# Performance work log

Hardware: AMD Instinct MI355X
Metric: run time of the kernel (lower is better)

Reference implementation:

```python
import jax, jax.numpy as jnp
import numpy as np

B, L, D = 8, 2048, 64

def setup_inputs() -> dict:
    key = jax.random.key(0)
    k1, k2 = jax.random.split(key)
    query = jax.random.normal(k1, (B, L, D), dtype=jnp.float32)
    key_t = jax.random.normal(k2, (B, L, D), dtype=jnp.float32)
    return {"query": query, "key": key_t}

def reference(query, key):
    d = query.shape[-1]
    # scores: [B, Lq, Lk] = Q K^T / sqrt(d)
    scores = jnp.einsum('bqd,bkd->bqk', query, key) / jnp.sqrt(jnp.asarray(d, query.dtype))
    weights = jax.nn.softmax(scores, axis=-1)  # dropout p=0.0 -> identity
    # output uses `key` as values, matching the original module
    return jnp.einsum('bqk,bkd->bqd', weights, key)
```

## Files before the change

### kernel.cpp

```cpp
#include <hip/hip_runtime.h>
#include <hip/hip_bf16.h>


#define LL 2048
#define DD 64
#define BQ 128
#define BK 64
#define KPAD 72
#define NSEG 8

typedef __attribute__((ext_vector_type(8))) short bf16x8;
typedef __attribute__((ext_vector_type(4))) float f32x4;

static __device__ __forceinline__ unsigned short f2bf(float f) {
  unsigned u = __builtin_bit_cast(unsigned, f);
  u += 0x7fffu + ((u >> 16) & 1u);
  return (unsigned short)(u >> 16);
}

__global__ __launch_bounds__(256, 4) void attn_kernel(
    const float* __restrict__ Q, const float* __restrict__ K,
    float* __restrict__ O, float* __restrict__ Opart,
    float* __restrict__ Lp, int seglen, int nseg) {
  __shared__ __attribute__((aligned(16))) unsigned short sKt[BK][KPAD];
  __shared__ __attribute__((aligned(16))) unsigned short sKtT[DD * KPAD];
  __shared__ __attribute__((aligned(16))) unsigned short sP[4][32][KPAD];

  const int tid  = threadIdx.x;
  const int wave = tid >> 6;
  const int lane = tid & 63;
  const int quad = lane >> 4;
  const int l16  = lane & 15;

  const int batch = blockIdx.y;
  const int seg   = blockIdx.z;
  const int q0w   = blockIdx.x * BQ + wave * 32;
  const int BLrows = gridDim.y * LL;

  const float qs = 0.125f * 1.44269504f;
  bf16x8 aq[2][2];
#pragma unroll
  for (int qb = 0; qb < 2; ++qb) {
    const float* qrow = Q + (size_t)(batch * LL + q0w + qb * 16 + l16) * DD;
#pragma unroll
    for (int ks = 0; ks < 2; ++ks) {
      const float* p = qrow + ks * 32 + quad * 8;
      float4 f0 = *(const float4*)(p);
      float4 f1 = *(const float4*)(p + 4);
      bf16x8 a;
      a[0] = (short)f2bf(f0.x * qs); a[1] = (short)f2bf(f0.y * qs);
      a[2] = (short)f2bf(f0.z * qs); a[3] = (short)f2bf(f0.w * qs);
      a[4] = (short)f2bf(f1.x * qs); a[5] = (short)f2bf(f1.y * qs);
      a[6] = (short)f2bf(f1.z * qs); a[7] = (short)f2bf(f1.w * qs);
      aq[qb][ks] = a;
    }
  }

  f32x4 oacc[2][4];
  float l_part[2][4];
#pragma unroll
  for (int qb = 0; qb < 2; ++qb) {
#pragma unroll
    for (int n = 0; n < 4; ++n) oacc[qb][n] = (f32x4){0.f, 0.f, 0.f, 0.f};
#pragma unroll
    for (int r = 0; r < 4; ++r) l_part[qb][r] = 0.f;
  }

  const int niter = seglen / BK;
  for (int t = 0; t < niter; ++t) {
    const int kv0 = seg * seglen + t * BK;
    __syncthreads();

    const float4* ksrc = (const float4*)(K + (size_t)(batch * LL + kv0) * DD);
#pragma unroll
    for (int i = 0; i < 2; ++i) {
      int p  = tid + i * 256;
      int kv = p >> 3;
      int a  = p & 7;
      float4 f0 = ksrc[p * 2];
      float4 f1 = ksrc[p * 2 + 1];
      unsigned short h[8];
      h[0] = f2bf(f0.x); h[1] = f2bf(f0.y); h[2] = f2bf(f0.z); h[3] = f2bf(f0.w);
      h[4] = f2bf(f1.x); h[5] = f2bf(f1.y); h[6] = f2bf(f1.z); h[7] = f2bf(f1.w);
      *(bf16x8*)&sKt[kv][a * 8] = *(const bf16x8*)h;
      int swz = (((kv >> 3) ^ a) & 7) * 8 + (kv & 7);
      unsigned short* dst = &sKtT[(a * 8) * KPAD + swz];
#pragma unroll
      for (int j = 0; j < 8; ++j) dst[j * KPAD] = h[j];
    }
    __syncthreads();

    f32x4 s0[4], s1[4];
#pragma unroll
    for (int n = 0; n < 4; ++n) {
      bf16x8 b0 = *(const bf16x8*)&sKt[n * 16 + l16][0 * 32 + quad * 8];
      bf16x8 b1 = *(const bf16x8*)&sKt[n * 16 + l16][1 * 32 + quad * 8];
      f32x4 z = (f32x4){0.f, 0.f, 0.f, 0.f};
      s0[n] = __builtin_amdgcn_mfma_f32_16x16x32_bf16(aq[0][0], b0, z, 0, 0, 0);
      s0[n] = __builtin_amdgcn_mfma_f32_16x16x32_bf16(aq[0][1], b1, s0[n], 0, 0, 0);
      s1[n] = __builtin_amdgcn_mfma_f32_16x16x32_bf16(aq[1][0], b0, z, 0, 0, 0);
      s1[n] = __builtin_amdgcn_mfma_f32_16x16x32_bf16(aq[1][1], b1, s1[n], 0, 0, 0);
    }

#pragma unroll
    for (int n = 0; n < 4; ++n) {
#pragma unroll
      for (int r = 0; r < 4; ++r) {
        float p0 = __builtin_amdgcn_exp2f(s0[n][r]);
        float p1 = __builtin_amdgcn_exp2f(s1[n][r]);
        l_part[0][r] += p0;
        l_part[1][r] += p1;
        sP[wave][quad * 4 + r][n * 16 + l16] = f2bf(p0);
        sP[wave][16 + quad * 4 + r][n * 16 + l16] = f2bf(p1);
      }
    }

#pragma unroll
    for (int ks = 0; ks < 2; ++ks) {
      bf16x8 a0 = *(const bf16x8*)&sP[wave][l16][ks * 32 + quad * 8];
      bf16x8 a1 = *(const bf16x8*)&sP[wave][16 + l16][ks * 32 + quad * 8];
#pragma unroll
      for (int n2 = 0; n2 < 4; ++n2) {
        int d = n2 * 16 + l16;
        bf16x8 b = *(const bf16x8*)&sKtT[d * KPAD + (((ks * 4 + quad) ^ (d >> 3)) & 7) * 8];
        oacc[0][n2] = __builtin_amdgcn_mfma_f32_16x16x32_bf16(a0, b, oacc[0][n2], 0, 0, 0);
        oacc[1][n2] = __builtin_amdgcn_mfma_f32_16x16x32_bf16(a1, b, oacc[1][n2], 0, 0, 0);
      }
    }
  }

#pragma unroll
  for (int qb = 0; qb < 2; ++qb)
#pragma unroll
    for (int r = 0; r < 4; ++r)
#pragma unroll
      for (int off = 1; off < 16; off <<= 1)
        l_part[qb][r] += __shfl_xor(l_part[qb][r], off);

  if (nseg == 1) {
#pragma unroll
    for (int qb = 0; qb < 2; ++qb)
#pragma unroll
      for (int r = 0; r < 4; ++r) {
        float invl = 1.0f / l_part[qb][r];
        float* orow = O + (size_t)(batch * LL + q0w + qb * 16 + quad * 4 + r) * DD;
#pragma unroll
        for (int n2 = 0; n2 < 4; ++n2)
          orow[n2 * 16 + l16] = oacc[qb][n2][r] * invl;
      }
  } else {
#pragma unroll
    for (int qb = 0; qb < 2; ++qb)
#pragma unroll
      for (int r = 0; r < 4; ++r) {
        int row = batch * LL + q0w + qb * 16 + quad * 4 + r;
        float* op = Opart + ((size_t)seg * BLrows + row) * DD;
#pragma unroll
        for (int n2 = 0; n2 < 4; ++n2)
          op[n2 * 16 + l16] = oacc[qb][n2][r];
        if (l16 == 0) Lp[seg * BLrows + row] = l_part[qb][r];
      }
  }
}

__global__ __launch_bounds__(256) void combine_kernel(
    const float* __restrict__ Opart, const float* __restrict__ Lp,
    float* __restrict__ O, int nseg, int BLrows) {
  const int tid = threadIdx.x;
  const int row = blockIdx.x * 4 + (tid >> 6);
  const int d   = tid & 63;
  float denom = 0.f, acc = 0.f;
  for (int s = 0; s < nseg; ++s) {
    denom += Lp[s * BLrows + row];
    acc   += Opart[((size_t)s * BLrows + row) * DD + d];
  }
  O[(size_t)row * DD + d] = acc / denom;
}

extern "C" void kernel_launch(void* const* d_in, const int* in_sizes, int n_in,
                              void* d_out, int out_size, void* d_ws, size_t ws_size,
                              hipStream_t stream) {
  const float* Q = (const float*)d_in[0];
  const float* K = (const float*)d_in[1];
  float* O = (float*)d_out;
  int B = in_sizes[0] / (LL * DD);
  int BLrows = B * LL;

  size_t need = ((size_t)NSEG * BLrows * DD + (size_t)NSEG * BLrows) * sizeof(float);
  if (ws_size >= need) {
    float* Opart = (float*)d_ws;
    float* Lpp = Opart + (size_t)NSEG * BLrows * DD;
    dim3 grid(LL / BQ, B, NSEG);
    attn_kernel<<<grid, 256, 0, stream>>>(Q, K, O, Opart, Lpp, LL / NSEG, NSEG);
    combine_kernel<<<dim3(BLrows / 4), 256, 0, stream>>>(Opart, Lpp, O, NSEG, BLrows);
  } else {
    dim3 grid(LL / BQ, B, 1);
    attn_kernel<<<grid, 256, 0, stream>>>(Q, K, O, nullptr, nullptr, LL, 1);
  }
}
```

Before: 91.56 us.

## Prefetch K tiles into registers, transpose score MFMA, store bf16 partials

Loads for the next K tile now go into registers while the current tile is being converted into shared memory, so global latency overlaps with compute. The score MFMA operands are swapped so each lane holds four consecutive keys for one query. This allows vectorized 8-byte writes of P to LDS and a cheaper row-sum reduction with only two shuffles. Split-K partial outputs are written as bf16 instead of fp32, halving the workspace traffic between the attention and combine kernels, at some cost in accuracy.

```diff
diff --git a/kernel.cpp b/kernel.cpp
--- a/kernel.cpp
+++ b/kernel.cpp
@@ -11,16 +11,21 @@
 
 typedef __attribute__((ext_vector_type(8))) short bf16x8;
 typedef __attribute__((ext_vector_type(4))) float f32x4;
+typedef __attribute__((ext_vector_type(4))) unsigned short u16x4;
 
 static __device__ __forceinline__ unsigned short f2bf(float f) {
   unsigned u = __builtin_bit_cast(unsigned, f);
   u += 0x7fffu + ((u >> 16) & 1u);
   return (unsigned short)(u >> 16);
 }
+static __device__ __forceinline__ float bf2f(unsigned short h) {
+  unsigned u = (unsigned)h << 16;
+  return __builtin_bit_cast(float, u);
+}
 
 __global__ __launch_bounds__(256, 4) void attn_kernel(
     const float* __restrict__ Q, const float* __restrict__ K,
-    float* __restrict__ O, float* __restrict__ Opart,
+    float* __restrict__ O, unsigned short* __restrict__ Opart,
     float* __restrict__ Lp, int seglen, int nseg) {
   __shared__ __attribute__((aligned(16))) unsigned short sKt[BK][KPAD];
   __shared__ __attribute__((aligned(16))) unsigned short sKtT[DD * KPAD];
@@ -38,10 +43,10 @@
   const int BLrows = gridDim.y * LL;
 
   const float qs = 0.125f * 1.44269504f;
-  bf16x8 aq[2][2];
-#pragma unroll
-  for (int qb = 0; qb < 2; ++qb) {
-    const float* qrow = Q + (size_t)(batch * LL + q0w + qb * 16 + l16) * DD;
+  bf16x8 bq[2][2];
+#pragma unroll
+  for (int qt = 0; qt < 2; ++qt) {
+    const float* qrow = Q + (size_t)(batch * LL + q0w + qt * 16 + l16) * DD;
 #pragma unroll
     for (int ks = 0; ks < 2; ++ks) {
       const float* p = qrow + ks * 32 + quad * 8;
@@ -52,66 +57,85 @@
       a[2] = (short)f2bf(f0.z * qs); a[3] = (short)f2bf(f0.w * qs);
       a[4] = (short)f2bf(f1.x * qs); a[5] = (short)f2bf(f1.y * qs);
       a[6] = (short)f2bf(f1.z * qs); a[7] = (short)f2bf(f1.w * qs);
-      aq[qb][ks] = a;
+      bq[qt][ks] = a;
     }
   }
 
   f32x4 oacc[2][4];
-  float l_part[2][4];
-#pragma unroll
-  for (int qb = 0; qb < 2; ++qb) {
-#pragma unroll
-    for (int n = 0; n < 4; ++n) oacc[qb][n] = (f32x4){0.f, 0.f, 0.f, 0.f};
-#pragma unroll
-    for (int r = 0; r < 4; ++r) l_part[qb][r] = 0.f;
+  float l_part[2];
+#pragma unroll
+  for (int qt = 0; qt < 2; ++qt) {
+#pragma unroll
+    for (int n = 0; n < 4; ++n) oacc[qt][n] = (f32x4){0.f, 0.f, 0.f, 0.f};
+    l_part[qt] = 0.f;
   }
 
   const int niter = seglen / BK;
+  const float4* kseg = (const float4*)(K + (size_t)(batch * LL + seg * seglen) * DD);
+
+  float4 pf[2][2];
+#pragma unroll
+  for (int i = 0; i < 2; ++i) {
+    int p = tid + i * 256;
+    pf[i][0] = kseg[p * 2];
+    pf[i][1] = kseg[p * 2 + 1];
+  }
+
   for (int t = 0; t < niter; ++t) {
-    const int kv0 = seg * seglen + t * BK;
     __syncthreads();
 
-    const float4* ksrc = (const float4*)(K + (size_t)(batch * LL + kv0) * DD);
 #pragma unroll
     for (int i = 0; i < 2; ++i) {
       int p  = tid + i * 256;
       int kv = p >> 3;
-      int a  = p & 7;
-      float4 f0 = ksrc[p * 2];
-      float4 f1 = ksrc[p * 2 + 1];
+      int oc = p & 7;
       unsigned short h[8];
-      h[0] = f2bf(f0.x); h[1] = f2bf(f0.y); h[2] = f2bf(f0.z); h[3] = f2bf(f0.w);
-      h[4] = f2bf(f1.x); h[5] = f2bf(f1.y); h[6] = f2bf(f1.z); h[7] = f2bf(f1.w);
-      *(bf16x8*)&sKt[kv][a * 8] = *(const bf16x8*)h;
-      int swz = (((kv >> 3) ^ a) & 7) * 8 + (kv & 7);
-      unsigned short* dst = &sKtT[(a * 8) * KPAD + swz];
+      h[0] = f2bf(pf[i][0].x); h[1] = f2bf(pf[i][0].y);
+      h[2] = f2bf(pf[i][0].z); h[3] = f2bf(pf[i][0].w);
+      h[4] = f2bf(pf[i][1].x); h[5] = f2bf(pf[i][1].y);
+      h[6] = f2bf(pf[i][1].z); h[7] = f2bf(pf[i][1].w);
+      *(bf16x8*)&sKt[kv][oc * 8] = *(const bf16x8*)h;
+      int swz = (((kv >> 3) ^ oc) & 7) * 8 + (kv & 7);
+      unsigned short* dst = &sKtT[(oc * 8) * KPAD + swz];
 #pragma unroll
       for (int j = 0; j < 8; ++j) dst[j * KPAD] = h[j];
     }
+
+    if (t + 1 < niter) {
+      const float4* ksrc = kseg + (t + 1) * (BK * DD / 4);
+#pragma unroll
+      for (int i = 0; i < 2; ++i) {
+        int p = tid + i * 256;
+        pf[i][0] = ksrc[p * 2];
+        pf[i][1] = ksrc[p * 2 + 1];
+      }
+    }
     __syncthreads();
 
-    f32x4 s0[4], s1[4];
-#pragma unroll
-    for (int n = 0; n < 4; ++n) {
-      bf16x8 b0 = *(const bf16x8*)&sKt[n * 16 + l16][0 * 32 + quad * 8];
-      bf16x8 b1 = *(const bf16x8*)&sKt[n * 16 + l16][1 * 32 + quad * 8];
+    f32x4 s[2][4];
+#pragma unroll
+    for (int mt = 0; mt < 4; ++mt) {
+      bf16x8 k0 = *(const bf16x8*)&sKt[mt * 16 + l16][quad * 8];
+      bf16x8 k1 = *(const bf16x8*)&sKt[mt * 16 + l16][32 + quad * 8];
       f32x4 z = (f32x4){0.f, 0.f, 0.f, 0.f};
-      s0[n] = __builtin_amdgcn_mfma_f32_16x16x32_bf16(aq[0][0], b0, z, 0, 0, 0);
-      s0[n] = __builtin_amdgcn_mfma_f32_16x16x32_bf16(aq[0][1], b1, s0[n], 0, 0, 0);
-      s1[n] = __builtin_amdgcn_mfma_f32_16x16x32_bf16(aq[1][0], b0, z, 0, 0, 0);
-      s1[n] = __builtin_amdgcn_mfma_f32_16x16x32_bf16(aq[1][1], b1, s1[n], 0, 0, 0);
-    }
-
-#pragma unroll
-    for (int n = 0; n < 4; ++n) {
-#pragma unroll
-      for (int r = 0; r < 4; ++r) {
-        float p0 = __builtin_amdgcn_exp2f(s0[n][r]);
-        float p1 = __builtin_amdgcn_exp2f(s1[n][r]);
-        l_part[0][r] += p0;
-        l_part[1][r] += p1;
-        sP[wave][quad * 4 + r][n * 16 + l16] = f2bf(p0);
-        sP[wave][16 + quad * 4 + r][n * 16 + l16] = f2bf(p1);
+      s[0][mt] = __builtin_amdgcn_mfma_f32_16x16x32_bf16(k0, bq[0][0], z, 0, 0, 0);
+      s[0][mt] = __builtin_amdgcn_mfma_f32_16x16x32_bf16(k1, bq[0][1], s[0][mt], 0, 0, 0);
+      s[1][mt] = __builtin_amdgcn_mfma_f32_16x16x32_bf16(k0, bq[1][0], z, 0, 0, 0);
+      s[1][mt] = __builtin_amdgcn_mfma_f32_16x16x32_bf16(k1, bq[1][1], s[1][mt], 0, 0, 0);
+    }
+
+#pragma unroll
+    for (int qt = 0; qt < 2; ++qt) {
+#pragma unroll
+      for (int mt = 0; mt < 4; ++mt) {
+        u16x4 h;
+#pragma unroll
+        for (int r = 0; r < 4; ++r) {
+          float p = __builtin_amdgcn_exp2f(s[qt][mt][r]);
+          l_part[qt] += p;
+          h[r] = f2bf(p);
+        }
+        *(u16x4*)&sP[wave][qt * 16 + l16][mt * 16 + quad * 4] = h;
       }
     }
 
@@ -120,51 +144,52 @@
       bf16x8 a0 = *(const bf16x8*)&sP[wave][l16][ks * 32 + quad * 8];
       bf16x8 a1 = *(const bf16x8*)&sP[wave][16 + l16][ks * 32 + quad * 8];
 #pragma unroll
-      for (int n2 = 0; n2 < 4; ++n2) {
-        int d = n2 * 16 + l16;
+      for (int nt = 0; nt < 4; ++nt) {
+        int d = nt * 16 + l16;
         bf16x8 b = *(const bf16x8*)&sKtT[d * KPAD + (((ks * 4 + quad) ^ (d >> 3)) & 7) * 8];
-        oacc[0][n2] = __builtin_amdgcn_mfma_f32_16x16x32_bf16(a0, b, oacc[0][n2], 0, 0, 0);
-        oacc[1][n2] = __builtin_amdgcn_mfma_f32_16x16x32_bf16(a1, b, oacc[1][n2], 0, 0, 0);
-      }
-    }
-  }
-
-#pragma unroll
-  for (int qb = 0; qb < 2; ++qb)
-#pragma unroll
-    for (int r = 0; r < 4; ++r)
-#pragma unroll
-      for (int off = 1; off < 16; off <<= 1)
-        l_part[qb][r] += __shfl_xor(l_part[qb][r], off);
+        oacc[0][nt] = __builtin_amdgcn_mfma_f32_16x16x32_bf16(a0, b, oacc[0][nt], 0, 0, 0);
+        oacc[1][nt] = __builtin_amdgcn_mfma_f32_16x16x32_bf16(a1, b, oacc[1][nt], 0, 0, 0);
+      }
+    }
+  }
+
+#pragma unroll
+  for (int qt = 0; qt < 2; ++qt) {
+    l_part[qt] += __shfl_xor(l_part[qt], 16);
+    l_part[qt] += __shfl_xor(l_part[qt], 32);
+  }
 
   if (nseg == 1) {
 #pragma unroll
-    for (int qb = 0; qb < 2; ++qb)
+    for (int qt = 0; qt < 2; ++qt)
 #pragma unroll
       for (int r = 0; r < 4; ++r) {
-        float invl = 1.0f / l_part[qb][r];
-        float* orow = O + (size_t)(batch * LL + q0w + qb * 16 + quad * 4 + r) * DD;
-#pragma unroll
-        for (int n2 = 0; n2 < 4; ++n2)
-          orow[n2 * 16 + l16] = oacc[qb][n2][r] * invl;
+        float lr = __shfl(l_part[qt], (lane & 48) | (quad * 4 + r), 64);
+        float invl = 1.0f / lr;
+        float* orow = O + (size_t)(batch * LL + q0w + qt * 16 + quad * 4 + r) * DD;
+#pragma unroll
+        for (int nt = 0; nt < 4; ++nt)
+          orow[nt * 16 + l16] = oacc[qt][nt][r] * invl;
       }
   } else {
 #pragma unroll
-    for (int qb = 0; qb < 2; ++qb)
+    for (int qt = 0; qt < 2; ++qt) {
+      if (quad == 0)
+        Lp[seg * BLrows + batch * LL + q0w + qt * 16 + l16] = l_part[qt];
 #pragma unroll
       for (int r = 0; r < 4; ++r) {
-        int row = batch * LL + q0w + qb * 16 + quad * 4 + r;
-        float* op = Opart + ((size_t)seg * BLrows + row) * DD;
-#pragma unroll
-        for (int n2 = 0; n2 < 4; ++n2)
-          op[n2 * 16 + l16] = oacc[qb][n2][r];
-        if (l16 == 0) Lp[seg * BLrows + row] = l_part[qb][r];
-      }
+        int row = batch * LL + q0w + qt * 16 + quad * 4 + r;
+        unsigned short* op = Opart + ((size_t)seg * BLrows + row) * DD;
+#pragma unroll
+        for (int nt = 0; nt < 4; ++nt)
+          op[nt * 16 + l16] = f2bf(oacc[qt][nt][r]);
+      }
+    }
   }
 }
 
 __global__ __launch_bounds__(256) void combine_kernel(
-    const float* __restrict__ Opart, const float* __restrict__ Lp,
+    const unsigned short* __restrict__ Opart, const float* __restrict__ Lp,
     float* __restrict__ O, int nseg, int BLrows) {
   const int tid = threadIdx.x;
   const int row = blockIdx.x * 4 + (tid >> 6);
@@ -172,7 +197,7 @@
   float denom = 0.f, acc = 0.f;
   for (int s = 0; s < nseg; ++s) {
     denom += Lp[s * BLrows + row];
-    acc   += Opart[((size_t)s * BLrows + row) * DD + d];
+    acc   += bf2f(Opart[((size_t)s * BLrows + row) * DD + d]);
   }
   O[(size_t)row * DD + d] = acc / denom;
 }
@@ -186,10 +211,11 @@
   int B = in_sizes[0] / (LL * DD);
   int BLrows = B * LL;
 
-  size_t need = ((size_t)NSEG * BLrows * DD + (size_t)NSEG * BLrows) * sizeof(float);
+  size_t need = (size_t)NSEG * BLrows * DD * sizeof(unsigned short) +
+                (size_t)NSEG * BLrows * sizeof(float);
   if (ws_size >= need) {
-    float* Opart = (float*)d_ws;
-    float* Lpp = Opart + (size_t)NSEG * BLrows * DD;
+    unsigned short* Opart = (unsigned short*)d_ws;
+    float* Lpp = (float*)(Opart + (size_t)NSEG * BLrows * DD);
     dim3 grid(LL / BQ, B, NSEG);
     attn_kernel<<<grid, 256, 0, stream>>>(Q, K, O, Opart, Lpp, LL / NSEG, NSEG);
     combine_kernel<<<dim3(BLrows / 4), 256, 0, stream>>>(Opart, Lpp, O, NSEG, BLrows);
```

New measurement: 92.29 us. About the same (+0.8%).
